# Kernel tuning notes

Measured on AMD Instinct MI355X. Metric: run time of the kernel, lower is better.

## Reference

```python
import jax, jax.numpy as jnp
import numpy as np

NEG_INF = -9e15


def setup_inputs() -> dict:
    key = jax.random.key(0)
    k1, k2, k3, k4, k5, k6 = jax.random.split(key, 6)
    B, N, F_IN, F_OUT = 16, 2048, 256, 128
    inputs = jax.random.normal(k1, (B, N, F_IN), dtype=jnp.float32)
    adj_matrix = jax.random.randint(k2, (B, N, N), 0, 2, dtype=jnp.int32)
    W = jax.random.normal(k3, (F_OUT, F_IN), dtype=jnp.float32) * (1.0 / np.sqrt(F_IN))
    b_W = jax.random.normal(k4, (F_OUT,), dtype=jnp.float32) * 0.02
    a = jax.random.normal(k5, (1, 2 * F_OUT), dtype=jnp.float32) * (1.0 / np.sqrt(2 * F_OUT))
    b_a = jax.random.normal(k6, (1,), dtype=jnp.float32) * 0.02
    return {"inputs": inputs, "adj_matrix": adj_matrix, "W": W, "b_W": b_W, "a": a, "b_a": b_a}


def reference(inputs, adj_matrix, W, b_W, a, b_a):
    # wh: [B, N, H]
    wh = jnp.einsum('bnf,hf->bnh', inputs, W) + b_W
    H = wh.shape[-1]
    # linear_self_W([wh_i, wh_j]) = a1.wh_i + a2.wh_j + b  (rank-1 linear over concat)
    a1 = a[0, :H]
    a2 = a[0, H:]
    src = jnp.einsum('bnh,h->bn', wh, a1)  # [B, N] contribution of row node i
    dst = jnp.einsum('bnh,h->bn', wh, a2)  # [B, N] contribution of col node j
    e = jax.nn.leaky_relu(src[:, :, None] + dst[:, None, :] + b_a[0], negative_slope=0.01)
    e = jnp.where(adj_matrix > 0, e, NEG_INF)
    att = jax.nn.softmax(e, axis=-1)  # dropout in eval mode = identity
    return jax.nn.elu(jnp.einsum('bij,bjh->bih', att, wh))
```

## Files before the change

### kernel.cpp

```cpp
#include <hip/hip_runtime.h>
#include <hip/hip_bf16.h>


#define BDIM 16
#define NDIM 2048
#define FIN 256
#define HDIM 128
#define LOG2E 1.4426950408889634f

typedef short short8 __attribute__((ext_vector_type(8)));
typedef float floatx4 __attribute__((ext_vector_type(4)));
typedef int intx4 __attribute__((ext_vector_type(4)));

__device__ __forceinline__ unsigned short f2bf(float x) {
    unsigned int u = __float_as_uint(x);
    unsigned int r = (u + 0x7fffu + ((u >> 16) & 1u)) >> 16;
    return (unsigned short)r;
}
__device__ __forceinline__ float bf2f(unsigned short s) {
    return __uint_as_float(((unsigned int)s) << 16);
}
__device__ __forceinline__ intx4 ldnt(const int* p) {
    return __builtin_nontemporal_load(reinterpret_cast<const intx4*>(p));
}

__global__ __launch_bounds__(256) void k_wh(const float* __restrict__ X,
                                            const float* __restrict__ W,
                                            const float* __restrict__ bW,
                                            const float* __restrict__ a,
                                            const float* __restrict__ ba_p,
                                            float* __restrict__ src,
                                            float* __restrict__ dst,
                                            unsigned short* __restrict__ whF) {
    __shared__ short lds[27648];
    short (*ah)[72] = (short(*)[72])lds;
    short (*al)[72] = (short(*)[72])(lds + 4608);
    short (*bh)[72] = (short(*)[72])(lds + 9216);
    short (*bl)[72] = (short(*)[72])(lds + 18432);
    short (*tb)[72] = (short(*)[72])lds;

    const int tid = threadIdx.x;
    const long row0 = (long)blockIdx.x * 64;
    const int w = tid >> 6, lane = tid & 63;
    const int lm = lane & 15, q = lane >> 4;
    const float ba0 = ba_p[0];

    float a1v[8], a2v[8], bwv[8];
    #pragma unroll
    for (int nt = 0; nt < 8; nt++) {
        a1v[nt] = a[nt * 16 + lm];
        a2v[nt] = a[HDIM + nt * 16 + lm];
        bwv[nt] = bW[nt * 16 + lm];
    }

    floatx4 acc[8];
    #pragma unroll
    for (int nt = 0; nt < 8; nt++) acc[nt] = (floatx4){0.f, 0.f, 0.f, 0.f};

    for (int k0 = 0; k0 < FIN; k0 += 64) {
        #pragma unroll
        for (int u = 0; u < 4; u++) {
            int idx = tid + u * 256;
            int r = idx >> 4, fc = (idx & 15) * 4;
            float4 v = *reinterpret_cast<const float4*>(X + (row0 + r) * FIN + k0 + fc);
            union { unsigned short s[4]; uint2 u2; } ph, pl;
            ph.s[0] = f2bf(v.x); pl.s[0] = f2bf(v.x - bf2f(ph.s[0]));
            ph.s[1] = f2bf(v.y); pl.s[1] = f2bf(v.y - bf2f(ph.s[1]));
            ph.s[2] = f2bf(v.z); pl.s[2] = f2bf(v.z - bf2f(ph.s[2]));
            ph.s[3] = f2bf(v.w); pl.s[3] = f2bf(v.w - bf2f(ph.s[3]));
            *reinterpret_cast<uint2*>(&ah[r][fc]) = ph.u2;
            *reinterpret_cast<uint2*>(&al[r][fc]) = pl.u2;
        }
        #pragma unroll
        for (int u = 0; u < 8; u++) {
            int idx = tid + u * 256;
            int hh = idx >> 4, fc = (idx & 15) * 4;
            float4 v = *reinterpret_cast<const float4*>(W + hh * FIN + k0 + fc);
            union { unsigned short s[4]; uint2 u2; } ph, pl;
            ph.s[0] = f2bf(v.x); pl.s[0] = f2bf(v.x - bf2f(ph.s[0]));
            ph.s[1] = f2bf(v.y); pl.s[1] = f2bf(v.y - bf2f(ph.s[1]));
            ph.s[2] = f2bf(v.z); pl.s[2] = f2bf(v.z - bf2f(ph.s[2]));
            ph.s[3] = f2bf(v.w); pl.s[3] = f2bf(v.w - bf2f(ph.s[3]));
            *reinterpret_cast<uint2*>(&bh[hh][fc]) = ph.u2;
            *reinterpret_cast<uint2*>(&bl[hh][fc]) = pl.u2;
        }
        __syncthreads();
        #pragma unroll
        for (int ks = 0; ks < 64; ks += 32) {
            short8 afh = *reinterpret_cast<const short8*>(&ah[w * 16 + lm][ks + q * 8]);
            short8 afl = *reinterpret_cast<const short8*>(&al[w * 16 + lm][ks + q * 8]);
            #pragma unroll
            for (int nt = 0; nt < 8; nt++) {
                short8 bfh = *reinterpret_cast<const short8*>(&bh[nt * 16 + lm][ks + q * 8]);
                short8 bfl = *reinterpret_cast<const short8*>(&bl[nt * 16 + lm][ks + q * 8]);
                acc[nt] = __builtin_amdgcn_mfma_f32_16x16x32_bf16(afh, bfh, acc[nt], 0, 0, 0);
                acc[nt] = __builtin_amdgcn_mfma_f32_16x16x32_bf16(afh, bfl, acc[nt], 0, 0, 0);
                acc[nt] = __builtin_amdgcn_mfma_f32_16x16x32_bf16(afl, bfh, acc[nt], 0, 0, 0);
            }
        }
        __syncthreads();
    }

    float s1[4] = {0.f, 0.f, 0.f, 0.f}, s2[4] = {0.f, 0.f, 0.f, 0.f};
    #pragma unroll
    for (int nt = 0; nt < 8; nt++) {
        #pragma unroll
        for (int r = 0; r < 4; r++) {
            float v = acc[nt][r] + bwv[nt];
            s1[r] += v * a1v[nt];
            s2[r] += v * a2v[nt];
            tb[nt * 16 + lm][w * 16 + q * 4 + r] = f2bf(v);
        }
    }
    #pragma unroll
    for (int r = 0; r < 4; r++) {
        #pragma unroll
        for (int o = 1; o < 16; o <<= 1) {
            s1[r] += __shfl_xor(s1[r], o);
            s2[r] += __shfl_xor(s2[r], o);
        }
    }
    if (lm == 0) {
        #pragma unroll
        for (int r = 0; r < 4; r++) {
            long row = row0 + w * 16 + q * 4 + r;
            src[row] = (s1[r] + ba0) * LOG2E;
            dst[row] = s2[r] * LOG2E;
        }
    }
    __syncthreads();
    const int b = (int)(row0 >> 11);
    const int jc0 = (int)((row0 & 2047) >> 5);
    const int f = tid >> 4;
    const int sub = tid & 15;
    const int jcrel = f >> 3, ht = f & 7;
    const size_t fbase = (((size_t)b * 64 + jc0 + jcrel) * 8 + ht) * 512;
    #pragma unroll
    for (int i = 0; i < 4; i++) {
        int l = sub * 4 + i;
        uint4 v = *reinterpret_cast<const uint4*>(&tb[ht * 16 + (l & 15)][jcrel * 32 + (l >> 4) * 8]);
        *reinterpret_cast<uint4*>(whF + fbase + l * 8) = v;
    }
}


#define BAR()                                                                  \
    do {                                                                       \
        asm volatile("s_waitcnt lgkmcnt(0)" ::: "memory");                     \
        __builtin_amdgcn_s_barrier();                                          \
    } while (0)

#define MD_PRE(PW1, BK, HI)                                                    \
    do {                                                                       \
        md[PW1][0] = maskB[BK][0 + (HI)][wrow];                                \
        md[PW1][1] = maskB[BK][2 + (HI)][wrow];                                \
        md[PW1][2] = maskB[BK][4 + (HI)][wrow];                                \
        md[PW1][3] = maskB[BK][6 + (HI)][wrow];                                \
    } while (0)

#define ADJ_ISSUE(GNEXT, H)                                                    \
    do {                                                                       \
        _Pragma("unroll")                                                      \
        for (int r = 0; r < 8; r++) {                                          \
            const int* ap = adj +                                              \
                (size_t)(rowbase + wave * 16 + (H) * 8 + r) * NDIM +           \
                (GNEXT) * 256 + lane * 4;                                      \
            av[r] = ldnt(ap);                                                  \
        }                                                                      \
    } while (0)

#define ADJ_BALLOT(GNEXT, H)                                                   \
    do {                                                                       \
        _Pragma("unroll")                                                      \
        for (int r = 0; r < 8; r++) {                                          \
            unsigned long long b0 = __ballot(av[r][0] != 0);                   \
            unsigned long long b1 = __ballot(av[r][1] != 0);                   \
            unsigned long long b2 = __ballot(av[r][2] != 0);                   \
            unsigned long long b3 = __ballot(av[r][3] != 0);                   \
            if (lane < 8) {                                                    \
                unsigned long long bb = (lane < 2) ? b0                        \
                                        : (lane < 4) ? b1                      \
                                        : (lane < 6) ? b2 : b3;                \
                unsigned wv = (lane & 1) ? (unsigned)(bb >> 32) : (unsigned)bb;\
                maskB[(GNEXT) & 1][lane][wave * 16 + (H) * 8 + r] = wv;        \
            }                                                                  \
        }                                                                      \
    } while (0)

#define CH(C)                                                                  \
    do {                                                                       \
        constexpr int PW = (C) & 1;                                            \
        const int T = g8 + (C);                                                \
        short8 s0, s1;                                                         \
        if (T < 63) {                 \
            const unsigned short* gp = gsrc + (size_t)(T + 1) * 4096;          \
            s0 = *reinterpret_cast<const short8*>(gp);                         \
            s1 = *reinterpret_cast<const short8*>(gp + 512);                   \
        }                                                                      \
        if ((C) == 0 && g8 < 56) ADJ_ISSUE((g8 >> 3) + 1, 0);                  \
        if ((C) == 3 && g8 < 56) {                                             \
            ADJ_BALLOT((g8 >> 3) + 1, 0);                                      \
            ADJ_ISSUE((g8 >> 3) + 1, 1);                                       \
        }                                                                      \
        if ((C) == 6 && g8 < 56) ADJ_BALLOT((g8 >> 3) + 1, 1);                 \
        if (T < 63) {       \
            d[PW ^ 1][0] =                                                     \
                *reinterpret_cast<const floatx4*>(&dstS[(T + 1) * 32 + q8]);   \
            d[PW ^ 1][1] =                                                     \
                *reinterpret_cast<const floatx4*>(&dstS[(T + 1) * 32 + q8 + 4]); \
            if ((C) < 7) {                                                     \
                MD_PRE(PW ^ 1, (g8 >> 3) & 1, (((C) + 1) & 4) ? 1 : 0);        \
            } else {                                                           \
                MD_PRE(PW ^ 1, ((g8 >> 3) + 1) & 1, 0);                        \
            }                                                                  \
        }                                                                      \
        const int base = 8 * ((C) & 3) + 2 * q;                                \
        short8 af;                                                             \
        _Pragma("unroll")                                                      \
        for (int j = 0; j < 8; j++) {                                          \
            float x = si + d[PW][j >> 2][j & 3];                               \
            x = fmaxf(x, 0.01f * x);               \
            float e2 = __builtin_amdgcn_exp2f(x);                              \
            unsigned bit = (md[PW][j & 3] >> (base + (j >> 2))) & 1u;          \
            float wgt = bit ? e2 : 0.f;                                        \
            lpart += wgt;                                                      \
            __hip_bfloat16 hb = __float2bfloat16(wgt);     \
            af[j] = *reinterpret_cast<short*>(&hb);                            \
        }                                                                      \
        _Pragma("unroll")                                                      \
        for (int hj = 0; hj < 8; hj++) {                                       \
            short8 fb = *reinterpret_cast<const short8*>(                      \
                &whS[PW][hj * 512 + lane * 8]);                                \
            acc[hj] = __builtin_amdgcn_mfma_f32_16x16x32_bf16(af, fb,          \
                                                              acc[hj], 0, 0, 0); \
        }                                                                      \
        if (T < 63) {          \
            *reinterpret_cast<short8*>(&whS[PW ^ 1][pofs]) = s0;               \
            *reinterpret_cast<short8*>(&whS[PW ^ 1][pofs + 512]) = s1;         \
        }                                                                      \
        BAR();                                                                 \
    } while (0)

__global__ __launch_bounds__(256) void k_attn(const int* __restrict__ adj,
                                              const unsigned short* __restrict__ whF,
                                              const float* __restrict__ src,
                                              const float* __restrict__ dst,
                                              float* __restrict__ out) {
    __shared__ short whS[2][4096];
    __shared__ unsigned maskB[2][8][65];
    __shared__ float dstS[2048];
    __shared__ float lred[64];
    __shared__ float linv_s[64];

    const int tid = threadIdx.x;
    const int bid = ((int)blockIdx.x & 7) * 64 + ((int)blockIdx.x >> 3);
    const int b = bid >> 5;
    const int i0 = (bid & 31) * 64;
    const int wave = tid >> 6, lane = tid & 63;
    const int lm = lane & 15, q = lane >> 4;
    const int q8 = q * 8;
    const int wrow = wave * 16 + lm;
    const int rowbase = b * NDIM + i0;

    const float si = src[rowbase + wrow];
    const unsigned short* gsrc =
        whF + (size_t)b * 262144 + wave * 1024 + lane * 8;
    const int pofs = wave * 1024 + lane * 8;

    floatx4 acc[8];
    #pragma unroll
    for (int hj = 0; hj < 8; hj++) acc[hj] = (floatx4){0.f, 0.f, 0.f, 0.f};
    float lpart = 0.f;

    unsigned md[2][4];
    floatx4 d[2][2];
    intx4 av[8];

    {
        const float* dg = dst + b * NDIM;
        *reinterpret_cast<float4*>(&dstS[tid * 8]) =
            *reinterpret_cast<const float4*>(dg + tid * 8);
        *reinterpret_cast<float4*>(&dstS[tid * 8 + 4]) =
            *reinterpret_cast<const float4*>(dg + tid * 8 + 4);
    }
    {
        short8 p0 = *reinterpret_cast<const short8*>(gsrc);
        short8 p1 = *reinterpret_cast<const short8*>(gsrc + 512);
        *reinterpret_cast<short8*>(&whS[0][pofs]) = p0;
        *reinterpret_cast<short8*>(&whS[0][pofs + 512]) = p1;
    }
    ADJ_ISSUE(0, 0);
    ADJ_BALLOT(0, 0);
    ADJ_ISSUE(0, 1);
    ADJ_BALLOT(0, 1);
    __syncthreads();
    MD_PRE(0, 0, 0);
    d[0][0] = *reinterpret_cast<const floatx4*>(&dstS[q8]);
    d[0][1] = *reinterpret_cast<const floatx4*>(&dstS[q8 + 4]);

    for (int g8 = 0; g8 < 64; g8 += 8) {
        CH(0); CH(1); CH(2); CH(3);
        CH(4); CH(5); CH(6); CH(7);
    }

    lpart += __shfl_xor(lpart, 16);
    lpart += __shfl_xor(lpart, 32);
    if (q == 0) lred[wrow] = lpart;
    __syncthreads();
    if (tid < 64) {
        float l = lred[tid];
        linv_s[tid] = l > 0.f ? 1.f / l : 0.f;
    }
    __syncthreads();

    #pragma unroll
    for (int r = 0; r < 4; r++) {
        int il = wave * 16 + q * 4 + r;
        float li = linv_s[il];
        size_t obase = ((size_t)(rowbase + il)) * HDIM + lm;
        #pragma unroll
        for (int hj = 0; hj < 8; hj++) {
            float x = acc[hj][r] * li;
            x = x > 0.f ? x : (__expf(x) - 1.f);
            out[obase + hj * 16] = x;
        }
    }
}

extern "C" void kernel_launch(void* const* d_in, const int* in_sizes, int n_in,
                              void* d_out, int out_size, void* d_ws, size_t ws_size,
                              hipStream_t stream) {
    const float* X  = (const float*)d_in[0];
    const int* adj  = (const int*)d_in[1];
    const float* W  = (const float*)d_in[2];
    const float* bW = (const float*)d_in[3];
    const float* a  = (const float*)d_in[4];
    const float* ba = (const float*)d_in[5];
    float* out = (float*)d_out;

    float* srcv = (float*)d_ws;
    float* dstv = srcv + BDIM * NDIM;
    unsigned short* whF = (unsigned short*)(dstv + BDIM * NDIM);

    k_wh<<<BDIM * NDIM / 64, 256, 0, stream>>>(X, W, bW, a, ba, srcv, dstv, whF);
    k_attn<<<BDIM * (NDIM / 64), 256, 0, stream>>>(adj, whF, srcv, dstv, out);
}
```

Before: 408.0 us.

## Process two key tiles per barrier with a four-slot shared memory ring

The main loop now handles two 32-column tiles per step, loading two tiles ahead into a four-buffer whS ring. This halves the number of block barriers. Mask and dst values are read from LDS just in time instead of being register-prefetched one step ahead. The cost is double the LDS for whS, more registers held across the larger global prefetch, and less latency hiding on the LDS reads for mask and dst.

```diff
diff --git a/kernel.cpp b/kernel.cpp
--- a/kernel.cpp
+++ b/kernel.cpp
@@ -150,14 +150,6 @@
         __builtin_amdgcn_s_barrier();                                          \
     } while (0)
 
-#define MD_PRE(PW1, BK, HI)                                                    \
-    do {                                                                       \
-        md[PW1][0] = maskB[BK][0 + (HI)][wrow];                                \
-        md[PW1][1] = maskB[BK][2 + (HI)][wrow];                                \
-        md[PW1][2] = maskB[BK][4 + (HI)][wrow];                                \
-        md[PW1][3] = maskB[BK][6 + (HI)][wrow];                                \
-    } while (0)
-
 #define ADJ_ISSUE(GNEXT, H)                                                    \
     do {                                                                       \
         _Pragma("unroll")                                                      \
@@ -187,56 +179,67 @@
         }                                                                      \
     } while (0)
 
-#define CH(C)                                                                  \
-    do {                                                                       \
-        constexpr int PW = (C) & 1;                                            \
-        const int T = g8 + (C);                                                \
-        short8 s0, s1;                                                         \
-        if (T < 63) {                 \
-            const unsigned short* gp = gsrc + (size_t)(T + 1) * 4096;          \
-            s0 = *reinterpret_cast<const short8*>(gp);                         \
-            s1 = *reinterpret_cast<const short8*>(gp + 512);                   \
-        }                                                                      \
-        if ((C) == 0 && g8 < 56) ADJ_ISSUE((g8 >> 3) + 1, 0);                  \
-        if ((C) == 3 && g8 < 56) {                                             \
-            ADJ_BALLOT((g8 >> 3) + 1, 0);                                      \
-            ADJ_ISSUE((g8 >> 3) + 1, 1);                                       \
-        }                                                                      \
-        if ((C) == 6 && g8 < 56) ADJ_BALLOT((g8 >> 3) + 1, 1);                 \
-        if (T < 63) {       \
-            d[PW ^ 1][0] =                                                     \
-                *reinterpret_cast<const floatx4*>(&dstS[(T + 1) * 32 + q8]);   \
-            d[PW ^ 1][1] =                                                     \
-                *reinterpret_cast<const floatx4*>(&dstS[(T + 1) * 32 + q8 + 4]); \
-            if ((C) < 7) {                                                     \
-                MD_PRE(PW ^ 1, (g8 >> 3) & 1, (((C) + 1) & 4) ? 1 : 0);        \
-            } else {                                                           \
-                MD_PRE(PW ^ 1, ((g8 >> 3) + 1) & 1, 0);                        \
-            }                                                                  \
-        }                                                                      \
+#define COMP(T, BUF, C)                                                        \
+    do {                                                                       \
+        const int hi = ((C) & 4) ? 1 : 0;                                      \
+        const int GB = (g8 >> 3) & 1;                                          \
+        unsigned m0 = maskB[GB][0 + hi][wrow];                                 \
+        unsigned m1 = maskB[GB][2 + hi][wrow];                                 \
+        unsigned m2 = maskB[GB][4 + hi][wrow];                                 \
+        unsigned m3 = maskB[GB][6 + hi][wrow];                                 \
+        floatx4 dd0 = *reinterpret_cast<const floatx4*>(&dstS[(T) * 32 + q8]); \
+        floatx4 dd1 =                                                          \
+            *reinterpret_cast<const floatx4*>(&dstS[(T) * 32 + q8 + 4]);       \
         const int base = 8 * ((C) & 3) + 2 * q;                                \
         short8 af;                                                             \
         _Pragma("unroll")                                                      \
         for (int j = 0; j < 8; j++) {                                          \
-            float x = si + d[PW][j >> 2][j & 3];                               \
+            float x = si + ((j >> 2) ? dd1[j & 3] : dd0[j & 3]);               \
             x = fmaxf(x, 0.01f * x);               \
             float e2 = __builtin_amdgcn_exp2f(x);                              \
-            unsigned bit = (md[PW][j & 3] >> (base + (j >> 2))) & 1u;          \
+            unsigned mw = (j & 3) == 0 ? m0 : (j & 3) == 1 ? m1                \
+                           : (j & 3) == 2 ? m2 : m3;                           \
+            unsigned bit = (mw >> (base + (j >> 2))) & 1u;                     \
             float wgt = bit ? e2 : 0.f;                                        \
             lpart += wgt;                                                      \
-            __hip_bfloat16 hb = __float2bfloat16(wgt);     \
+            __hip_bfloat16 hb = __float2bfloat16(wgt);        \
             af[j] = *reinterpret_cast<short*>(&hb);                            \
         }                                                                      \
         _Pragma("unroll")                                                      \
         for (int hj = 0; hj < 8; hj++) {                                       \
             short8 fb = *reinterpret_cast<const short8*>(                      \
-                &whS[PW][hj * 512 + lane * 8]);                                \
+                &whS[BUF][hj * 512 + lane * 8]);                               \
             acc[hj] = __builtin_amdgcn_mfma_f32_16x16x32_bf16(af, fb,          \
                                                               acc[hj], 0, 0, 0); \
         }                                                                      \
-        if (T < 63) {          \
-            *reinterpret_cast<short8*>(&whS[PW ^ 1][pofs]) = s0;               \
-            *reinterpret_cast<short8*>(&whS[PW ^ 1][pofs + 512]) = s1;         \
+    } while (0)
+
+#define PAIR(PI)                                                               \
+    do {                                                                       \
+        const int T = g8 + (PI) * 2;                                           \
+        constexpr int BUF0 = ((PI) & 1) * 2;                                   \
+        constexpr int WBUF = ((((PI) & 1)) ^ 1) * 2;                           \
+        short8 s0, s1, s2, s3;                                                 \
+        if (T + 2 < 64) {       \
+            const unsigned short* gp = gsrc + (size_t)(T + 2) * 4096;          \
+            s0 = *reinterpret_cast<const short8*>(gp);                         \
+            s1 = *reinterpret_cast<const short8*>(gp + 512);                   \
+            s2 = *reinterpret_cast<const short8*>(gp + 4096);                  \
+            s3 = *reinterpret_cast<const short8*>(gp + 4096 + 512);            \
+        }                                                                      \
+        if ((PI) == 0 && g8 < 56) ADJ_ISSUE((g8 >> 3) + 1, 0);                 \
+        if ((PI) == 1 && g8 < 56) {                                            \
+            ADJ_BALLOT((g8 >> 3) + 1, 0);                                      \
+            ADJ_ISSUE((g8 >> 3) + 1, 1);                                       \
+        }                                                                      \
+        if ((PI) == 3 && g8 < 56) ADJ_BALLOT((g8 >> 3) + 1, 1);                \
+        COMP(T, BUF0, (PI) * 2);                                               \
+        COMP(T + 1, BUF0 + 1, (PI) * 2 + 1);                                   \
+        if (T + 2 < 64) {    \
+            *reinterpret_cast<short8*>(&whS[WBUF][pofs]) = s0;                 \
+            *reinterpret_cast<short8*>(&whS[WBUF][pofs + 512]) = s1;           \
+            *reinterpret_cast<short8*>(&whS[WBUF + 1][pofs]) = s2;             \
+            *reinterpret_cast<short8*>(&whS[WBUF + 1][pofs + 512]) = s3;       \
         }                                                                      \
         BAR();                                                                 \
     } while (0)
@@ -246,7 +249,7 @@
                                               const float* __restrict__ src,
                                               const float* __restrict__ dst,
                                               float* __restrict__ out) {
-    __shared__ short whS[2][4096];
+    __shared__ short whS[4][4096];
     __shared__ unsigned maskB[2][8][65];
     __shared__ float dstS[2048];
     __shared__ float lred[64];
@@ -272,8 +275,6 @@
     for (int hj = 0; hj < 8; hj++) acc[hj] = (floatx4){0.f, 0.f, 0.f, 0.f};
     float lpart = 0.f;
 
-    unsigned md[2][4];
-    floatx4 d[2][2];
     intx4 av[8];
 
     {
@@ -286,21 +287,21 @@
     {
         short8 p0 = *reinterpret_cast<const short8*>(gsrc);
         short8 p1 = *reinterpret_cast<const short8*>(gsrc + 512);
+        short8 p2 = *reinterpret_cast<const short8*>(gsrc + 4096);
+        short8 p3 = *reinterpret_cast<const short8*>(gsrc + 4096 + 512);
         *reinterpret_cast<short8*>(&whS[0][pofs]) = p0;
         *reinterpret_cast<short8*>(&whS[0][pofs + 512]) = p1;
+        *reinterpret_cast<short8*>(&whS[1][pofs]) = p2;
+        *reinterpret_cast<short8*>(&whS[1][pofs + 512]) = p3;
     }
     ADJ_ISSUE(0, 0);
     ADJ_BALLOT(0, 0);
     ADJ_ISSUE(0, 1);
     ADJ_BALLOT(0, 1);
     __syncthreads();
-    MD_PRE(0, 0, 0);
-    d[0][0] = *reinterpret_cast<const floatx4*>(&dstS[q8]);
-    d[0][1] = *reinterpret_cast<const floatx4*>(&dstS[q8 + 4]);
 
     for (int g8 = 0; g8 < 64; g8 += 8) {
-        CH(0); CH(1); CH(2); CH(3);
-        CH(4); CH(5); CH(6); CH(7);
+        PAIR(0); PAIR(1); PAIR(2); PAIR(3);
     }
 
     lpart += __shfl_xor(lpart, 16);
```

New measurement: 397.7 us. -2.5%, faster.
